# Kernel tuning notes

Hardware: AMD Instinct MI355X
Metric: run time of the kernel (lower is better)

The kernel has to match this reference:

```python
import jax, jax.numpy as jnp
import numpy as np
from jax.scipy.special import gammaln, betaln

B, S, F, D, FEAT = 8, 128, 512, 256, 80


def conv1d(x, w, b, pad):
    # x: (B, C_in, L), w: (C_out, C_in, K) -> (B, C_out, L)
    y = jax.lax.conv_general_dilated(x, w, window_strides=(1,), padding=[(pad, pad)],
                                     dimension_numbers=('NCH', 'OIH', 'NCH'))
    return y + b[None, :, None]


def beta_binomial_log_prior(token_length, feat_length):
    # Vectorized betabinom(n=L-1, a=j+1, b=F_len-j).logpmf(k) over (B, S, F).
    k = jnp.arange(S, dtype=jnp.float32)[None, :, None]
    j = jnp.arange(F, dtype=jnp.float32)[None, None, :]
    L = token_length.astype(jnp.float32)[:, None, None]
    Fl = feat_length.astype(jnp.float32)[:, None, None]
    valid = (k < L) & (j < Fl)
    n = jnp.maximum(L - 1.0, 0.0)
    ks = jnp.minimum(k, n)                 # clamp outside-support k (masked anyway)
    a = j + 1.0                            # omega=1: a = i, i = j+1
    b = jnp.maximum(Fl - j, 1.0)           # b = F_len - i + 1 = F_len - j
    log_binom = gammaln(n + 1.0) - gammaln(ks + 1.0) - gammaln(n - ks + 1.0)
    lp = log_binom + betaln(ks + a, n - ks + b) - betaln(a, b)
    return jnp.where(valid, lp, -jnp.inf)


def setup_inputs() -> dict:
    key = jax.random.key(0)
    ks = jax.random.split(key, 10)
    h = jax.random.normal(ks[0], (B, S, D), jnp.float32)
    m = jax.random.normal(ks[1], (B, F, FEAT), jnp.float32)
    token_length = jax.random.randint(ks[2], (B,), S // 2, S + 1, dtype=jnp.int32)
    feat_length = jax.random.randint(ks[3], (B,), F // 2, F + 1, dtype=jnp.int32)
    mask = jnp.arange(S)[None, :] < token_length[:, None]
    w = lambda k, sh: jax.random.normal(k, sh, jnp.float32) * 0.02
    return dict(
        h=h, m=m,
        tw1=w(ks[4], (D, D, 3)), tb1=jnp.zeros((D,), jnp.float32),
        tw2=w(ks[5], (D, D, 1)), tb2=jnp.zeros((D,), jnp.float32),
        fw1=w(ks[6], (D, FEAT, 3)), fb1=jnp.zeros((D,), jnp.float32),
        fw2=w(ks[7], (D, D, 3)), fb2=jnp.zeros((D,), jnp.float32),
        fw3=w(ks[8], (D, D, 1)), fb3=jnp.zeros((D,), jnp.float32),
        mask=mask, token_length=token_length, feat_length=feat_length,
    )


def reference(h, m, tw1, tb1, tw2, tb2, fw1, fb1, fw2, fb2, fw3, fb3,
              mask, token_length, feat_length):
    # text conv stack: conv3(relu) -> conv1
    x = conv1d(h.transpose(0, 2, 1), tw1, tb1, 1)
    x = conv1d(jax.nn.relu(x), tw2, tb2, 0)
    hh = x.transpose(0, 2, 1)              # (B, S, D)
    # feat conv stack: conv3(relu) -> conv3(relu) -> conv1
    y = conv1d(m.transpose(0, 2, 1), fw1, fb1, 1)
    y = conv1d(jax.nn.relu(y), fw2, fb2, 1)
    y = conv1d(jax.nn.relu(y), fw3, fb3, 0)
    mm = y.transpose(0, 2, 1)              # (B, F, D)
    # broadcasted L2 pairwise distance -> (B, S, F)
    diff = hh[:, :, None, :] - mm[:, None, :, :]
    dist = jnp.sqrt(jnp.sum(diff * diff, axis=-1))
    logit = jnp.where(mask[:, :, None], -dist, -jnp.inf)
    log_a_soft = jax.nn.log_softmax(logit, axis=1)
    log_prior = beta_binomial_log_prior(token_length, feat_length)
    return log_prior + log_a_soft
```

## Files before the change

### kernel.cpp

```cpp
#include <hip/hip_runtime.h>
#include <cmath>

constexpr int B = 8, S = 128, F = 512, D = 256, FEAT = 80;
#define NEG_HUGE (-3.0e38f)

typedef unsigned short u16;
typedef unsigned int u32;
typedef __attribute__((ext_vector_type(8))) short bf16x8;
typedef __attribute__((ext_vector_type(4))) float f32x4;

#define MFMA(a, b, c) __builtin_amdgcn_mfma_f32_16x16x32_bf16((a), (b), (c), 0, 0, 0)

__device__ __forceinline__ u16 f2bf(float x) {
    u32 u = __float_as_uint(x);
    return (u16)((u + 0x7fffu + ((u >> 16) & 1u)) >> 16);
}
__device__ __forceinline__ float bf2f(u16 s) {
    return __uint_as_float(((u32)s) << 16);
}

constexpr int PRF = F + 2;
constexpr int PRH = S + 2;
constexpr int CIN_M = 96;

constexpr int N_G   = 1024;
constexpr int N_WT1 = 256 * 768;
constexpr int N_WT2 = 256 * 256;
constexpr int N_WF1 = 256 * 288;
constexpr int N_WF2 = 256 * 768;
constexpr int N_WF3 = 256 * 256;
constexpr int N_Y1P = B * 2 * D;
constexpr int PREP_TOTAL = N_G + N_WT1 + N_WT2 + N_WF1 + N_WF2 + N_WF3 + N_Y1P;

__device__ __forceinline__ void wconv_frag(const float* __restrict__ w,
                                           u16* __restrict__ o16,
                                           int I, int TAPS, int CINP, int idx) {
    int KSTEPS = TAPS * CINP / 32;
    int e    = idx & 7;
    int lane = (idx >> 3) & 63;
    int rest = idx >> 9;
    int kb   = rest % KSTEPS;
    int ct16 = rest / KSTEPS;
    int co = ct16 * 16 + (lane & 15);
    int k  = kb * 32 + (lane >> 4) * 8 + e;
    int tap = k / CINP, ci = k % CINP;
    float v = (ci < I) ? w[(co * I + ci) * TAPS + tap] : 0.f;
    o16[idx] = f2bf(v);
}

__global__ __launch_bounds__(256) void k_prep(
    const float* __restrict__ tw1, const float* __restrict__ tw2,
    const float* __restrict__ fw1, const float* __restrict__ fw2,
    const float* __restrict__ fw3,
    float* __restrict__ gt,
    u16* __restrict__ WT1, u16* __restrict__ WT2,
    u16* __restrict__ WF1, u16* __restrict__ WF2, u16* __restrict__ WF3,
    u16* __restrict__ Y1)
{
    int idx = blockIdx.x * 256 + threadIdx.x;
    if (idx < N_G) { gt[idx] = (float)lgamma((double)idx); return; }
    idx -= N_G;
    if (idx < N_WT1) { wconv_frag(tw1, WT1, 256, 3, 256, idx); return; }
    idx -= N_WT1;
    if (idx < N_WT2) { wconv_frag(tw2, WT2, 256, 1, 256, idx); return; }
    idx -= N_WT2;
    if (idx < N_WF1) { wconv_frag(fw1, WF1,  80, 3, CIN_M, idx); return; }
    idx -= N_WF1;
    if (idx < N_WF2) { wconv_frag(fw2, WF2, 256, 3, 256, idx); return; }
    idx -= N_WF2;
    if (idx < N_WF3) { wconv_frag(fw3, WF3, 256, 1, 256, idx); return; }
    idx -= N_WF3;
    if (idx < N_Y1P) {
        int ci = idx % D;
        int which = (idx / D) & 1;
        int b = idx / (2 * D);
        int row = b * PRF + (which ? (PRF - 1) : 0);
        Y1[row * D + ci] = 0;
    }
}

constexpr int SHBYTES = 17408;

template<int CINP, int TAPS, bool RELU, int MODE>
__device__ __forceinline__ void conv_block(
    char* shbuf,
    const u16* __restrict__ A, int arowbase,
    const float* __restrict__ src, int b, int p0,
    const u16* __restrict__ Wf, const float* __restrict__ bias, int co0,
    u16* __restrict__ O, int orowbase)
{
    constexpr int KTOT = TAPS * CINP;
    constexpr int KSTEPS = KTOT / 32;
    constexpr int KPT = CINP / 32;
    constexpr int ITER = (KSTEPS + 3) / 4;
    constexpr int ROWS = 32 + TAPS - 1;
    constexpr int RB = CINP * 2;
    constexpr int G8 = CINP / 8;

    const int t  = threadIdx.x;
    const int w  = t >> 6;
    const int l  = t & 63;
    const int lr = l & 15;
    const int kg = l >> 4;

    for (int c = t; c < ROWS * G8; c += 256) {
        int row = c / G8, cc = c % G8;
        bf16x8 v;
        if constexpr (MODE == 0) {
            v = *(const bf16x8*)(A + (arowbase + row) * CINP + cc * 8);
        } else {
            constexpr int LIMIT = (MODE == 1) ? F : S;
            constexpr int SSTR  = (MODE == 1) ? FEAT : D;
            int pr = p0 + row;
            bool valid = (pr >= 1) && (pr <= LIMIT) && (MODE == 2 || cc < FEAT / 8);
            if (valid) {
                const float* sp = src + ((size_t)(b * LIMIT + (pr - 1))) * SSTR + cc * 8;
                float4 x0 = *(const float4*)sp;
                float4 x1 = *(const float4*)(sp + 4);
                v[0] = (short)f2bf(x0.x); v[1] = (short)f2bf(x0.y);
                v[2] = (short)f2bf(x0.z); v[3] = (short)f2bf(x0.w);
                v[4] = (short)f2bf(x1.x); v[5] = (short)f2bf(x1.y);
                v[6] = (short)f2bf(x1.z); v[7] = (short)f2bf(x1.w);
            } else {
                v = bf16x8{0, 0, 0, 0, 0, 0, 0, 0};
            }
        }
        *(bf16x8*)(shbuf + row * RB + ((cc * 16) ^ ((row & 7) << 4))) = v;
    }
    __syncthreads();

    f32x4 a00 = {0.f, 0.f, 0.f, 0.f}, a01 = a00, a10 = a00, a11 = a00;
    const u16* wp0 = Wf + (size_t)(co0 >> 4) * KSTEPS * 512 + l * 8;
    const u16* wp1 = wp0 + (size_t)KSTEPS * 512;

#pragma unroll
    for (int i = 0; i < ITER; ++i) {
        int kb = w + 4 * i;
        if (KSTEPS % 4 == 0 || kb < KSTEPS) {
            int colb = (kb % KPT) * 64 + kg * 16;
            int rr0 = lr + kb / KPT;
            int rr1 = rr0 + 16;
            bf16x8 ah0 = *(const bf16x8*)(shbuf + rr0 * RB + (colb ^ ((rr0 & 7) << 4)));
            bf16x8 ah1 = *(const bf16x8*)(shbuf + rr1 * RB + (colb ^ ((rr1 & 7) << 4)));
            bf16x8 b0  = *(const bf16x8*)(wp0 + kb * 512);
            bf16x8 b1  = *(const bf16x8*)(wp1 + kb * 512);
            a00 = MFMA(ah0, b0, a00);
            a01 = MFMA(ah0, b1, a01);
            a10 = MFMA(ah1, b0, a10);
            a11 = MFMA(ah1, b1, a11);
        }
    }
    __syncthreads();

    float (*red)[64][17] = (float(*)[64][17])shbuf;
#pragma unroll
    for (int r = 0; r < 4; ++r) {
        red[w][l][0 * 4 + r] = a00[r];
        red[w][l][1 * 4 + r] = a01[r];
        red[w][l][2 * 4 + r] = a10[r];
        red[w][l][3 * 4 + r] = a11[r];
    }
    __syncthreads();

#pragma unroll
    for (int j = 0; j < 4; ++j) {
        int v = w * 4 + j;
        float s = red[0][l][v] + red[1][l][v] + red[2][l][v] + red[3][l][v];
        int m2 = v >> 3, ct = (v >> 2) & 1, r = v & 3;
        int co = co0 + ct * 16 + lr;
        int orow = orowbase + m2 * 16 + kg * 4 + r;
        float val = s + bias[co];
        if (RELU) val = fmaxf(val, 0.f);
        O[orow * 256 + co] = f2bf(val);
    }
}

__global__ __launch_bounds__(256) void k_convA(
    const float* __restrict__ m, const float* __restrict__ h,
    const u16* __restrict__ WF1, const u16* __restrict__ WT1,
    const float* __restrict__ fb1, const float* __restrict__ tb1,
    u16* __restrict__ Y1, u16* __restrict__ X1)
{
    __shared__ __align__(16) char shbuf[SHBYTES];
    int bid = blockIdx.x;
    if (bid < 1024) {
        int co0 = (bid & 7) * 32;
        int p0  = ((bid >> 3) & 15) * 32;
        int b   = bid >> 7;
        conv_block<CIN_M, 3, true, 1>(shbuf, nullptr, 0, m, b, p0,
                                      WF1, fb1, co0, Y1, b * PRF + p0 + 1);
    } else {
        int i = bid - 1024;
        int co0 = (i & 7) * 32;
        int p0  = ((i >> 3) & 3) * 32;
        int b   = i >> 5;
        conv_block<D, 3, true, 2>(shbuf, nullptr, 0, h, b, p0,
                                  WT1, tb1, co0, X1, b * S + p0);
    }
}

__global__ __launch_bounds__(256) void k_convB(
    const u16* __restrict__ Y1, const u16* __restrict__ X1,
    const u16* __restrict__ WF2, const u16* __restrict__ WT2,
    const float* __restrict__ fb2, const float* __restrict__ tb2,
    u16* __restrict__ Y2, u16* __restrict__ Ho)
{
    __shared__ __align__(16) char shbuf[SHBYTES];
    int bid = blockIdx.x;
    if (bid < 1024) {
        int co0 = (bid & 7) * 32;
        int p0  = ((bid >> 3) & 15) * 32;
        int b   = bid >> 7;
        conv_block<D, 3, true, 0>(shbuf, Y1, b * PRF + p0, nullptr, 0, 0,
                                  WF2, fb2, co0, Y2, b * F + p0);
    } else {
        int i = bid - 1024;
        int co0 = (i & 7) * 32;
        int p0  = ((i >> 3) & 3) * 32;
        int b   = i >> 5;
        conv_block<D, 1, false, 0>(shbuf, X1, b * S + p0, nullptr, 0, 0,
                                   WT2, tb2, co0, Ho, b * S + p0);
    }
}

__global__ __launch_bounds__(512) void k_distsoft(
    const u16* __restrict__ Y2, const u16* __restrict__ Ho,
    const u16* __restrict__ WF3, const float* __restrict__ fb3,
    const float* __restrict__ gt,
    const int* __restrict__ tokl, const int* __restrict__ featl,
    float* __restrict__ out)
{
    __shared__ float gts[1024];
    __shared__ __align__(16) u16 hol[128 * 256];
    __shared__ u16 mo[16 * 256];
    __shared__ float sc[128][18];
    __shared__ float red[512];
    __shared__ float na[128], nb[16], mcol[16], scol[16];
    int t = threadIdx.x;
    int b = blockIdx.x >> 5;
    int f0 = (blockIdx.x & 31) * 16;
    for (int i = t; i < 1024; i += 512) gts[i] = gt[i];
    int L = tokl[b], Fl = featl[b];

    int w = t >> 6, l = t & 63, lr = l & 15, kg = (l >> 4) & 3;

    for (int c = t; c < 128 * 32; c += 512) {
        int row = c >> 5, cc = c & 31;
        bf16x8 v = *(const bf16x8*)(Ho + (b * S + row) * 256 + cc * 8);
        *(bf16x8*)((char*)hol + row * 512 + ((cc * 16) ^ ((row & 7) << 4))) = v;
    }

    {
        f32x4 acc0 = {0.f, 0.f, 0.f, 0.f}, acc1 = acc0;
        const u16* ap = Y2 + (b * F + f0 + lr) * 256 + kg * 8;
        const u16* wp = WF3 + (size_t)(2 * w) * 8 * 512 + l * 8;
#pragma unroll
        for (int kb = 0; kb < 8; ++kb) {
            bf16x8 av = *(const bf16x8*)(ap + kb * 32);
            bf16x8 b0 = *(const bf16x8*)(wp + kb * 512);
            bf16x8 b1 = *(const bf16x8*)(wp + (8 + kb) * 512);
            acc0 = MFMA(av, b0, acc0);
            acc1 = MFMA(av, b1, acc1);
        }
#pragma unroll
        for (int nt = 0; nt < 2; ++nt) {
            int co = w * 32 + nt * 16 + lr;
            float bv = fb3[co];
            const f32x4& a = nt == 0 ? acc0 : acc1;
#pragma unroll
            for (int r = 0; r < 4; ++r) {
                int pos = kg * 4 + r;
                int byte = pos * 512 + ((co * 2) ^ ((pos & 7) << 4));
                *(u16*)((char*)mo + byte) = f2bf(a[r] + bv);
            }
        }
    }
    __syncthreads();

    {
        int c = t >> 5;
        int byte = c * 512 + (((t & 31) * 16) ^ ((c & 7) << 4));
        bf16x8 v = *(const bf16x8*)((char*)mo + byte);
        float s = 0.f;
#pragma unroll
        for (int e = 0; e < 8; ++e) { float a = bf2f((u16)v[e]); s = fmaf(a, a, s); }
        red[t] = s;
    }
    __syncthreads();
    if (t < 16) {
        float s = 0.f;
#pragma unroll
        for (int j = 0; j < 32; ++j) s += red[t * 32 + j];
        nb[t] = s;
    }
    __syncthreads();

    {
        int r = t >> 2;
        int x = (r & 7) << 4;
        float s = 0.f;
#pragma unroll
        for (int j = 0; j < 8; ++j) {
            int byte = r * 512 + ((((t & 3) * 128) + j * 16) ^ x);
            bf16x8 v = *(const bf16x8*)((char*)hol + byte);
#pragma unroll
            for (int e = 0; e < 8; ++e) { float a = bf2f((u16)v[e]); s = fmaf(a, a, s); }
        }
        red[t] = s;
    }
    __syncthreads();
    if (t < 128) na[t] = red[4 * t] + red[4 * t + 1] + red[4 * t + 2] + red[4 * t + 3];

    f32x4 acc = {0.f, 0.f, 0.f, 0.f};
    {
        int rr = w * 16 + lr;
        const char* abase = (const char*)hol + rr * 512;
        int ax = (rr & 7) << 4;
        const char* bbase = (const char*)mo + lr * 512;
        int bx = (lr & 7) << 4;
#pragma unroll
        for (int kb = 0; kb < 8; ++kb) {
            int colb = kg * 16 + kb * 64;
            bf16x8 a0 = *(const bf16x8*)(abase + (colb ^ ax));
            bf16x8 bv = *(const bf16x8*)(bbase + (colb ^ bx));
            acc = MFMA(a0, bv, acc);
        }
    }
    __syncthreads();
#pragma unroll
    for (int r = 0; r < 4; ++r) {
        int sl = w * 16 + kg * 4 + r;
        float d2 = na[sl] + nb[lr] - 2.f * acc[r];
        sc[sl][lr] = -sqrtf(fmaxf(d2, 0.f));
    }
    __syncthreads();

    int fi = t & 15, sg = t >> 4;
    float sv[4], mx = -INFINITY;
#pragma unroll
    for (int i = 0; i < 4; ++i) {
        int s = sg + i * 32;
        float v = sc[s][fi];
        if (s >= L) v = -INFINITY;
        sv[i] = v;
        mx = fmaxf(mx, v);
    }
    red[t] = mx;
    __syncthreads();
    if (t < 16) {
        float m2 = -INFINITY;
#pragma unroll
        for (int j = 0; j < 32; ++j) m2 = fmaxf(m2, red[j * 16 + t]);
        mcol[t] = m2;
    }
    __syncthreads();
    float m = mcol[fi];
    float sum = 0.f;
#pragma unroll
    for (int i = 0; i < 4; ++i) sum += expf(sv[i] - m);
    red[t] = sum;
    __syncthreads();
    if (t < 16) {
        float s = 0.f;
#pragma unroll
        for (int j = 0; j < 32; ++j) s += red[j * 16 + t];
        scol[t] = s;
    }
    __syncthreads();
    float lse = m + logf(scol[fi]);

    int f = f0 + fi;
    float cb = gts[L] - gts[L + Fl] + gts[Fl + 1];
    bool fvalid = f < Fl;
    float cf = fvalid ? (-gts[f + 1] - gts[Fl - f]) : 0.f;
#pragma unroll
    for (int i = 0; i < 4; ++i) {
        int s = sg + i * 32;
        float o;
        if (s >= L || !fvalid) {
            o = NEG_HUGE;
        } else {
            float lp = cb + cf - gts[s + 1] - gts[L - s]
                     + gts[s + f + 1] + gts[L - 1 - s + Fl - f];
            o = lp + sv[i] - lse;
        }
        out[(b * S + s) * F + f] = o;
    }
}

extern "C" void kernel_launch(void* const* d_in, const int* in_sizes, int n_in,
                              void* d_out, int out_size, void* d_ws, size_t ws_size,
                              hipStream_t stream)
{
    const float* h   = (const float*)d_in[0];
    const float* m_  = (const float*)d_in[1];
    const float* tw1 = (const float*)d_in[2];
    const float* tb1 = (const float*)d_in[3];
    const float* tw2 = (const float*)d_in[4];
    const float* tb2 = (const float*)d_in[5];
    const float* fw1 = (const float*)d_in[6];
    const float* fb1 = (const float*)d_in[7];
    const float* fw2 = (const float*)d_in[8];
    const float* fb2 = (const float*)d_in[9];
    const float* fw3 = (const float*)d_in[10];
    const float* fb3 = (const float*)d_in[11];
    const int* tokl  = (const int*)d_in[13];
    const int* featl = (const int*)d_in[14];

    char* base = (char*)d_ws;
    size_t off = 0;
    auto alloc = [&](size_t bytes) -> char* {
        size_t a = (off + 255) & ~(size_t)255;
        off = a + bytes;
        return base + a;
    };

    float* gt = (float*)alloc(N_G * 4);
    u16* WT1 = (u16*)alloc(N_WT1 * 2);
    u16* WT2 = (u16*)alloc(N_WT2 * 2);
    u16* WF1 = (u16*)alloc(N_WF1 * 2);
    u16* WF2 = (u16*)alloc(N_WF2 * 2);
    u16* WF3 = (u16*)alloc(N_WF3 * 2);
    u16* Y1  = (u16*)alloc((size_t)B * PRF * D * 2);
    u16* Y2  = (u16*)alloc((size_t)B * F * D * 2);
    u16* X1  = (u16*)alloc((size_t)B * S * D * 2);
    u16* Ho  = (u16*)alloc((size_t)B * S * D * 2);
    float* out = (float*)d_out;

    k_prep<<<(PREP_TOTAL + 255) / 256, 256, 0, stream>>>(
        tw1, tw2, fw1, fw2, fw3, gt, WT1, WT2, WF1, WF2, WF3, Y1);

    k_convA<<<1280, 256, 0, stream>>>(m_, h, WF1, WT1, fb1, tb1, Y1, X1);
    k_convB<<<1280, 256, 0, stream>>>(Y1, X1, WF2, WT2, fb2, tb2, Y2, Ho);
    k_distsoft<<<B * (F / 16), 512, 0, stream>>>(Y2, Ho, WF3, fb3, gt,
                                                 tokl, featl, out);
}
```

Before: 34.70 us.

## Use 8 waves per conv block and drop the lgamma table and Y1 padding prep

The conv blocks go from 256 to 512 threads, so the K-steps are split across 8 waves instead of 4 and the cross-wave reduction sums over 8 partials. This cuts the serial MFMA chain per wave but doubles the shared-memory reduction buffer. The lgamma table is no longer built in the prep kernel; each distsoft block now computes it itself in double precision, which repeats that work in every block. The zeroing of the Y1 padding rows is dropped and replaced by a bounds check when convB loads its input tile (new MODE 3).

```diff
diff --git a/kernel.cpp b/kernel.cpp
--- a/kernel.cpp
+++ b/kernel.cpp
@@ -23,14 +23,12 @@
 constexpr int PRH = S + 2;
 constexpr int CIN_M = 96;
 
-constexpr int N_G   = 1024;
 constexpr int N_WT1 = 256 * 768;
 constexpr int N_WT2 = 256 * 256;
 constexpr int N_WF1 = 256 * 288;
 constexpr int N_WF2 = 256 * 768;
 constexpr int N_WF3 = 256 * 256;
-constexpr int N_Y1P = B * 2 * D;
-constexpr int PREP_TOTAL = N_G + N_WT1 + N_WT2 + N_WF1 + N_WF2 + N_WF3 + N_Y1P;
+constexpr int PREP_TOTAL = N_WT1 + N_WT2 + N_WF1 + N_WF2 + N_WF3;
 
 __device__ __forceinline__ void wconv_frag(const float* __restrict__ w,
                                            u16* __restrict__ o16,
@@ -52,14 +50,10 @@
     const float* __restrict__ tw1, const float* __restrict__ tw2,
     const float* __restrict__ fw1, const float* __restrict__ fw2,
     const float* __restrict__ fw3,
-    float* __restrict__ gt,
     u16* __restrict__ WT1, u16* __restrict__ WT2,
-    u16* __restrict__ WF1, u16* __restrict__ WF2, u16* __restrict__ WF3,
-    u16* __restrict__ Y1)
+    u16* __restrict__ WF1, u16* __restrict__ WF2, u16* __restrict__ WF3)
 {
     int idx = blockIdx.x * 256 + threadIdx.x;
-    if (idx < N_G) { gt[idx] = (float)lgamma((double)idx); return; }
-    idx -= N_G;
     if (idx < N_WT1) { wconv_frag(tw1, WT1, 256, 3, 256, idx); return; }
     idx -= N_WT1;
     if (idx < N_WT2) { wconv_frag(tw2, WT2, 256, 1, 256, idx); return; }
@@ -69,17 +63,9 @@
     if (idx < N_WF2) { wconv_frag(fw2, WF2, 256, 3, 256, idx); return; }
     idx -= N_WF2;
     if (idx < N_WF3) { wconv_frag(fw3, WF3, 256, 1, 256, idx); return; }
-    idx -= N_WF3;
-    if (idx < N_Y1P) {
-        int ci = idx % D;
-        int which = (idx / D) & 1;
-        int b = idx / (2 * D);
-        int row = b * PRF + (which ? (PRF - 1) : 0);
-        Y1[row * D + ci] = 0;
-    }
-}
-
-constexpr int SHBYTES = 17408;
+}
+
+constexpr int SHBYTES = 8 * 64 * 17 * 4;
 
 template<int CINP, int TAPS, bool RELU, int MODE>
 __device__ __forceinline__ void conv_block(
@@ -92,7 +78,7 @@
     constexpr int KTOT = TAPS * CINP;
     constexpr int KSTEPS = KTOT / 32;
     constexpr int KPT = CINP / 32;
-    constexpr int ITER = (KSTEPS + 3) / 4;
+    constexpr int ITER = (KSTEPS + 7) / 8;
     constexpr int ROWS = 32 + TAPS - 1;
     constexpr int RB = CINP * 2;
     constexpr int G8 = CINP / 8;
@@ -103,11 +89,17 @@
     const int lr = l & 15;
     const int kg = l >> 4;
 
-    for (int c = t; c < ROWS * G8; c += 256) {
+    for (int c = t; c < ROWS * G8; c += 512) {
         int row = c / G8, cc = c % G8;
         bf16x8 v;
         if constexpr (MODE == 0) {
             v = *(const bf16x8*)(A + (arowbase + row) * CINP + cc * 8);
+        } else if constexpr (MODE == 3) {
+            int pr = p0 + row;
+            if (pr >= 1 && pr <= F)
+                v = *(const bf16x8*)(A + (arowbase + row) * CINP + cc * 8);
+            else
+                v = bf16x8{0, 0, 0, 0, 0, 0, 0, 0};
         } else {
             constexpr int LIMIT = (MODE == 1) ? F : S;
             constexpr int SSTR  = (MODE == 1) ? FEAT : D;
@@ -135,8 +127,8 @@
 
 #pragma unroll
     for (int i = 0; i < ITER; ++i) {
-        int kb = w + 4 * i;
-        if (KSTEPS % 4 == 0 || kb < KSTEPS) {
+        int kb = w + 8 * i;
+        if (KSTEPS % 8 == 0 || kb < KSTEPS) {
             int colb = (kb % KPT) * 64 + kg * 16;
             int rr0 = lr + kb / KPT;
             int rr1 = rr0 + 16;
@@ -163,9 +155,11 @@
     __syncthreads();
 
 #pragma unroll
-    for (int j = 0; j < 4; ++j) {
-        int v = w * 4 + j;
-        float s = red[0][l][v] + red[1][l][v] + red[2][l][v] + red[3][l][v];
+    for (int j = 0; j < 2; ++j) {
+        int v = w * 2 + j;
+        float s = 0.f;
+#pragma unroll
+        for (int ww = 0; ww < 8; ++ww) s += red[ww][l][v];
         int m2 = v >> 3, ct = (v >> 2) & 1, r = v & 3;
         int co = co0 + ct * 16 + lr;
         int orow = orowbase + m2 * 16 + kg * 4 + r;
@@ -175,7 +169,7 @@
     }
 }
 
-__global__ __launch_bounds__(256) void k_convA(
+__global__ __launch_bounds__(512) void k_convA(
     const float* __restrict__ m, const float* __restrict__ h,
     const u16* __restrict__ WF1, const u16* __restrict__ WT1,
     const float* __restrict__ fb1, const float* __restrict__ tb1,
@@ -199,7 +193,7 @@
     }
 }
 
-__global__ __launch_bounds__(256) void k_convB(
+__global__ __launch_bounds__(512) void k_convB(
     const u16* __restrict__ Y1, const u16* __restrict__ X1,
     const u16* __restrict__ WF2, const u16* __restrict__ WT2,
     const float* __restrict__ fb2, const float* __restrict__ tb2,
@@ -211,7 +205,7 @@
         int co0 = (bid & 7) * 32;
         int p0  = ((bid >> 3) & 15) * 32;
         int b   = bid >> 7;
-        conv_block<D, 3, true, 0>(shbuf, Y1, b * PRF + p0, nullptr, 0, 0,
+        conv_block<D, 3, true, 3>(shbuf, Y1, b * PRF + p0, nullptr, 0, p0,
                                   WF2, fb2, co0, Y2, b * F + p0);
     } else {
         int i = bid - 1024;
@@ -226,7 +220,6 @@
 __global__ __launch_bounds__(512) void k_distsoft(
     const u16* __restrict__ Y2, const u16* __restrict__ Ho,
     const u16* __restrict__ WF3, const float* __restrict__ fb3,
-    const float* __restrict__ gt,
     const int* __restrict__ tokl, const int* __restrict__ featl,
     float* __restrict__ out)
 {
@@ -239,7 +232,7 @@
     int t = threadIdx.x;
     int b = blockIdx.x >> 5;
     int f0 = (blockIdx.x & 31) * 16;
-    for (int i = t; i < 1024; i += 512) gts[i] = gt[i];
+    for (int i = t; i < 1024; i += 512) gts[i] = (float)lgamma((double)i);
     int L = tokl[b], Fl = featl[b];
 
     int w = t >> 6, l = t & 63, lr = l & 15, kg = (l >> 4) & 3;
@@ -415,7 +408,6 @@
         return base + a;
     };
 
-    float* gt = (float*)alloc(N_G * 4);
     u16* WT1 = (u16*)alloc(N_WT1 * 2);
     u16* WT2 = (u16*)alloc(N_WT2 * 2);
     u16* WF1 = (u16*)alloc(N_WF1 * 2);
@@ -428,10 +420,10 @@
     float* out = (float*)d_out;
 
     k_prep<<<(PREP_TOTAL + 255) / 256, 256, 0, stream>>>(
-        tw1, tw2, fw1, fw2, fw3, gt, WT1, WT2, WF1, WF2, WF3, Y1);
-
-    k_convA<<<1280, 256, 0, stream>>>(m_, h, WF1, WT1, fb1, tb1, Y1, X1);
-    k_convB<<<1280, 256, 0, stream>>>(Y1, X1, WF2, WT2, fb2, tb2, Y2, Ho);
-    k_distsoft<<<B * (F / 16), 512, 0, stream>>>(Y2, Ho, WF3, fb3, gt,
+        tw1, tw2, fw1, fw2, fw3, WT1, WT2, WF1, WF2, WF3);
+
+    k_convA<<<1280, 512, 0, stream>>>(m_, h, WF1, WT1, fb1, tb1, Y1, X1);
+    k_convB<<<1280, 512, 0, stream>>>(Y1, X1, WF2, WT2, fb2, tb2, Y2, Ho);
+    k_distsoft<<<B * (F / 16), 512, 0, stream>>>(Y2, Ho, WF3, fb3,
                                                  tokl, featl, out);
 }
```

New measurement: 35.92 us. 3.5% more time.

## Widen conv block output-channel tile to 64 to reuse staged activations

Applied to the files above, without the earlier changes.

Each conv block now computes 64 output channels instead of 32, with eight accumulators per warp, and the grid for both conv kernels is halved. Each activation tile staged in shared memory and each A-fragment read from LDS now feeds twice as many MFMAs, which cuts redundant input loads and bf16 conversion. The cross-warp reduction is split into two passes through shared memory. Costs are higher register pressure, fewer blocks (640) to fill the GPU, and an extra pair of syncs in the epilogue.

```diff
diff --git a/kernel.cpp b/kernel.cpp
--- a/kernel.cpp
+++ b/kernel.cpp
@@ -129,11 +129,15 @@
     }
     __syncthreads();
 
-    f32x4 a00 = {0.f, 0.f, 0.f, 0.f}, a01 = a00, a10 = a00, a11 = a00;
-    const u16* wp0 = Wf + (size_t)(co0 >> 4) * KSTEPS * 512 + l * 8;
-    const u16* wp1 = wp0 + (size_t)KSTEPS * 512;
-
-#pragma unroll
+    f32x4 acc0[4], acc1[4];
+#pragma unroll
+    for (int ct = 0; ct < 4; ++ct) {
+        acc0[ct] = f32x4{0.f, 0.f, 0.f, 0.f};
+        acc1[ct] = f32x4{0.f, 0.f, 0.f, 0.f};
+    }
+    const u16* wp = Wf + (size_t)(co0 >> 4) * KSTEPS * 512 + l * 8;
+
+#pragma unroll 2
     for (int i = 0; i < ITER; ++i) {
         int kb = w + 4 * i;
         if (KSTEPS % 4 == 0 || kb < KSTEPS) {
@@ -142,36 +146,36 @@
             int rr1 = rr0 + 16;
             bf16x8 ah0 = *(const bf16x8*)(shbuf + rr0 * RB + (colb ^ ((rr0 & 7) << 4)));
             bf16x8 ah1 = *(const bf16x8*)(shbuf + rr1 * RB + (colb ^ ((rr1 & 7) << 4)));
-            bf16x8 b0  = *(const bf16x8*)(wp0 + kb * 512);
-            bf16x8 b1  = *(const bf16x8*)(wp1 + kb * 512);
-            a00 = MFMA(ah0, b0, a00);
-            a01 = MFMA(ah0, b1, a01);
-            a10 = MFMA(ah1, b0, a10);
-            a11 = MFMA(ah1, b1, a11);
-        }
-    }
-    __syncthreads();
+#pragma unroll
+            for (int ct = 0; ct < 4; ++ct) {
+                bf16x8 bv = *(const bf16x8*)(wp + ((size_t)ct * KSTEPS + kb) * 512);
+                acc0[ct] = MFMA(ah0, bv, acc0[ct]);
+                acc1[ct] = MFMA(ah1, bv, acc1[ct]);
+            }
+        }
+    }
 
     float (*red)[64][17] = (float(*)[64][17])shbuf;
 #pragma unroll
-    for (int r = 0; r < 4; ++r) {
-        red[w][l][0 * 4 + r] = a00[r];
-        red[w][l][1 * 4 + r] = a01[r];
-        red[w][l][2 * 4 + r] = a10[r];
-        red[w][l][3 * 4 + r] = a11[r];
-    }
-    __syncthreads();
-
-#pragma unroll
-    for (int j = 0; j < 4; ++j) {
-        int v = w * 4 + j;
-        float s = red[0][l][v] + red[1][l][v] + red[2][l][v] + red[3][l][v];
-        int m2 = v >> 3, ct = (v >> 2) & 1, r = v & 3;
-        int co = co0 + ct * 16 + lr;
-        int orow = orowbase + m2 * 16 + kg * 4 + r;
-        float val = s + bias[co];
-        if (RELU) val = fmaxf(val, 0.f);
-        O[orow * 256 + co] = f2bf(val);
+    for (int p = 0; p < 2; ++p) {
+        __syncthreads();
+#pragma unroll
+        for (int ct = 0; ct < 4; ++ct)
+#pragma unroll
+            for (int r = 0; r < 4; ++r)
+                red[w][l][ct * 4 + r] = p == 0 ? acc0[ct][r] : acc1[ct][r];
+        __syncthreads();
+#pragma unroll
+        for (int j = 0; j < 4; ++j) {
+            int v = w * 4 + j;
+            float s = red[0][l][v] + red[1][l][v] + red[2][l][v] + red[3][l][v];
+            int ct = v >> 2, r = v & 3;
+            int co = co0 + ct * 16 + lr;
+            int orow = orowbase + p * 16 + kg * 4 + r;
+            float val = s + bias[co];
+            if (RELU) val = fmaxf(val, 0.f);
+            O[orow * 256 + co] = f2bf(val);
+        }
     }
 }
 
@@ -183,17 +187,17 @@
 {
     __shared__ __align__(16) char shbuf[SHBYTES];
     int bid = blockIdx.x;
-    if (bid < 1024) {
-        int co0 = (bid & 7) * 32;
-        int p0  = ((bid >> 3) & 15) * 32;
-        int b   = bid >> 7;
+    if (bid < 512) {
+        int co0 = (bid & 3) * 64;
+        int p0  = ((bid >> 2) & 15) * 32;
+        int b   = bid >> 6;
         conv_block<CIN_M, 3, true, 1>(shbuf, nullptr, 0, m, b, p0,
                                       WF1, fb1, co0, Y1, b * PRF + p0 + 1);
     } else {
-        int i = bid - 1024;
-        int co0 = (i & 7) * 32;
-        int p0  = ((i >> 3) & 3) * 32;
-        int b   = i >> 5;
+        int i = bid - 512;
+        int co0 = (i & 3) * 64;
+        int p0  = ((i >> 2) & 3) * 32;
+        int b   = i >> 4;
         conv_block<D, 3, true, 2>(shbuf, nullptr, 0, h, b, p0,
                                   WT1, tb1, co0, X1, b * S + p0);
     }
@@ -207,17 +211,17 @@
 {
     __shared__ __align__(16) char shbuf[SHBYTES];
     int bid = blockIdx.x;
-    if (bid < 1024) {
-        int co0 = (bid & 7) * 32;
-        int p0  = ((bid >> 3) & 15) * 32;
-        int b   = bid >> 7;
+    if (bid < 512) {
+        int co0 = (bid & 3) * 64;
+        int p0  = ((bid >> 2) & 15) * 32;
+        int b   = bid >> 6;
         conv_block<D, 3, true, 0>(shbuf, Y1, b * PRF + p0, nullptr, 0, 0,
                                   WF2, fb2, co0, Y2, b * F + p0);
     } else {
-        int i = bid - 1024;
-        int co0 = (i & 7) * 32;
-        int p0  = ((i >> 3) & 3) * 32;
-        int b   = i >> 5;
+        int i = bid - 512;
+        int co0 = (i & 3) * 64;
+        int p0  = ((i >> 2) & 3) * 32;
+        int b   = i >> 4;
         conv_block<D, 1, false, 0>(shbuf, X1, b * S + p0, nullptr, 0, 0,
                                    WT2, tb2, co0, Ho, b * S + p0);
     }
@@ -430,8 +434,8 @@
     k_prep<<<(PREP_TOTAL + 255) / 256, 256, 0, stream>>>(
         tw1, tw2, fw1, fw2, fw3, gt, WT1, WT2, WF1, WF2, WF3, Y1);
 
-    k_convA<<<1280, 256, 0, stream>>>(m_, h, WF1, WT1, fb1, tb1, Y1, X1);
-    k_convB<<<1280, 256, 0, stream>>>(Y1, X1, WF2, WT2, fb2, tb2, Y2, Ho);
+    k_convA<<<640, 256, 0, stream>>>(m_, h, WF1, WT1, fb1, tb1, Y1, X1);
+    k_convB<<<640, 256, 0, stream>>>(Y1, X1, WF2, WT2, fb2, tb2, Y2, Ho);
     k_distsoft<<<B * (F / 16), 512, 0, stream>>>(Y2, Ho, WF3, fb3, gt,
                                                  tokl, featl, out);
 }
```

Result: slower. 36.85 us (+6.2%).
